# Optimization experiments

Hardware: AMD Instinct MI355X
Metric: run time of the kernel (lower is better)

Reference implementation:

```python
import jax, jax.numpy as jnp
import numpy as np

N_X, N_NEIGH, D_IN, D_HID, D_OUT = 8192, 8192, 512, 32, 256
NEG_BIG = -9.0e15


def setup_inputs() -> dict:
    key = jax.random.key(0)
    ks = jax.random.split(key, 16)
    s_in = 1.0 / np.sqrt(D_IN)
    s_hid = 1.0 / np.sqrt(D_HID)
    return {
        "x": jax.random.normal(ks[0], (N_X, D_IN), jnp.float32),
        "neigh": jax.random.normal(ks[1], (N_NEIGH, D_IN), jnp.float32),
        "adj": jax.random.randint(ks[2], (N_X, N_NEIGH), 0, 2, jnp.int32),
        # att_x MLP: Linear(D_IN,D_HID) -> tanh -> Linear(D_HID,D_HID)
        "Wx1": jax.random.uniform(ks[3], (D_IN, D_HID), jnp.float32, -s_in, s_in),
        "bx1": jnp.zeros((D_HID,), jnp.float32),
        "Wx2": jax.random.uniform(ks[4], (D_HID, D_HID), jnp.float32, -s_hid, s_hid),
        "bx2": jnp.zeros((D_HID,), jnp.float32),
        # att_neigh MLP
        "Wn1": jax.random.uniform(ks[5], (D_IN, D_HID), jnp.float32, -s_in, s_in),
        "bn1": jnp.zeros((D_HID,), jnp.float32),
        "Wn2": jax.random.uniform(ks[6], (D_HID, D_HID), jnp.float32, -s_hid, s_hid),
        "bn2": jnp.zeros((D_HID,), jnp.float32),
        # fc_value, fc_x
        "Wv": jax.random.uniform(ks[7], (D_IN, D_OUT), jnp.float32, -s_in, s_in),
        "bv": jnp.zeros((D_OUT,), jnp.float32),
        "Wfx": jax.random.uniform(ks[8], (D_IN, D_OUT), jnp.float32, -s_in, s_in),
        "bfx": jnp.zeros((D_OUT,), jnp.float32),
    }


def reference(x, neigh, adj, Wx1, bx1, Wx2, bx2, Wn1, bn1, Wn2, bn2, Wv, bv, Wfx, bfx):
    # eval mode: dropouts are identity. edge_emb gather in original is dead code.
    neib_att = jnp.tanh(neigh @ Wn1 + bn1) @ Wn2 + bn2      # (N_neigh, H)
    value = neigh @ Wv + bv                                  # (N_neigh, D_OUT)
    x_att = jnp.tanh(x @ Wx1 + bx1) @ Wx2 + bx2              # (N_x, H)
    ws = jnp.einsum("nh,mh->nm", x_att, neib_att)            # (N_x, N_neigh)
    ws = jax.nn.leaky_relu(ws, negative_slope=0.01)
    ws = jnp.where(adj > 0, ws, jnp.float32(NEG_BIG))
    ws = jax.nn.softmax(ws, axis=1)
    agg_neib = ws @ value                                    # (N_x, D_OUT)
    out = jnp.concatenate([x @ Wfx + bfx, agg_neib], axis=1)  # (N_x, 2*D_OUT)
    return out
```

## Files before the change

### kernel.cpp

```cpp
#include <hip/hip_runtime.h>
#include <hip/hip_bf16.h>

#define NX 8192
#define NN 8192
#define DIN 512
#define DHID 32
#define DOUT 256

typedef __bf16 bf16x8 __attribute__((ext_vector_type(8)));
typedef float f32x4 __attribute__((ext_vector_type(4)));
typedef unsigned short u16x8 __attribute__((ext_vector_type(8)));

__device__ __forceinline__ unsigned short f2bf(float f) {
  __hip_bfloat16 h = __float2bfloat16(f);
  return __builtin_bit_cast(unsigned short, h);
}
__device__ __forceinline__ float bf2f(unsigned short u) {
  unsigned int v = ((unsigned int)u) << 16;
  return __builtin_bit_cast(float, v);
}
__device__ __forceinline__ f32x4 mfma16(u16x8 a, u16x8 b, f32x4 c) {
  return __builtin_amdgcn_mfma_f32_16x16x32_bf16(
      __builtin_bit_cast(bf16x8, a), __builtin_bit_cast(bf16x8, b), c, 0, 0, 0);
}
__device__ __forceinline__ u16x8 cvt8(float4 a0, float4 a1) {
  u16x8 u;
  u[0] = f2bf(a0.x); u[1] = f2bf(a0.y); u[2] = f2bf(a0.z); u[3] = f2bf(a0.w);
  u[4] = f2bf(a1.x); u[5] = f2bf(a1.y); u[6] = f2bf(a1.z); u[7] = f2bf(a1.w);
  return u;
}

__global__ __launch_bounds__(256) void k_wt(
    const float* __restrict__ Wv, const float* __restrict__ Wfx,
    const float* __restrict__ Wx1, const float* __restrict__ Wn1,
    const float* __restrict__ Wx2, const float* __restrict__ Wn2,
    unsigned short* __restrict__ WvT, unsigned short* __restrict__ WfxT,
    unsigned short* __restrict__ Wx1T, unsigned short* __restrict__ Wn1T,
    unsigned short* __restrict__ Wx2T, unsigned short* __restrict__ Wn2T) {
  const float* src; unsigned short* dst; int K, C;
  switch (blockIdx.y) {
    case 0:  src = Wv;  dst = WvT;  K = DIN; C = 256; break;
    case 1:  src = Wfx; dst = WfxT; K = DIN; C = 256; break;
    case 2:  src = Wx1; dst = Wx1T; K = DIN; C = 32;  break;
    case 3:  src = Wn1; dst = Wn1T; K = DIN; C = 32;  break;
    case 4:  src = Wx2; dst = Wx2T; K = 32;  C = 32;  break;
    default: src = Wn2; dst = Wn2T; K = 32;  C = 32;  break;
  }
  int tc = C >> 5, tk = K >> 5;
  if ((int)blockIdx.x >= tc * tk) return;
  int ik = blockIdx.x / tc, ic = blockIdx.x % tc;
  __shared__ float tile[32][33];
  int t = threadIdx.x, tx = t & 31, ty0 = t >> 5;
  #pragma unroll
  for (int q = 0; q < 4; ++q) {
    int ty = ty0 + q * 8;
    tile[ty][tx] = src[(ik * 32 + ty) * C + ic * 32 + tx];
  }
  __syncthreads();
  #pragma unroll
  for (int q = 0; q < 4; ++q) {
    int ty = ty0 + q * 8;
    dst[(ic * 32 + ty) * K + ik * 32 + tx] = f2bf(tile[tx][ty]);
  }
}

__global__ __launch_bounds__(256) void k_prep(
    const float* __restrict__ x, const float* __restrict__ neigh,
    const float* __restrict__ bfx, const float* __restrict__ bv,
    const float* __restrict__ bx1, const float* __restrict__ bn1,
    const unsigned short* __restrict__ WfxT, const unsigned short* __restrict__ WvT,
    const unsigned short* __restrict__ Wx1T, const unsigned short* __restrict__ Wn1T,
    float* __restrict__ out, unsigned short* __restrict__ Vp,
    unsigned short* __restrict__ Hx, unsigned short* __restrict__ Hn) {
  int job = blockIdx.y;
  const float* A = job ? neigh : x;
  const float* bias = job ? bv : bfx;
  const float* b1 = job ? bn1 : bx1;
  const unsigned short* WT = job ? WvT : WfxT;
  const unsigned short* W1T = job ? Wn1T : Wx1T;
  unsigned short* H = job ? Hn : Hx;
  __shared__ __align__(16) char As[2][64 * 64];
  int t = threadIdx.x;
  int lane = t & 63, w = t >> 6;
  int r = lane & 15, h4 = lane >> 4;
  int bm = blockIdx.x * 64;
  f32x4 acc[4][4];
  f32x4 acch[4];
  #pragma unroll
  for (int i = 0; i < 4; ++i) {
    acch[i] = (f32x4){0.f, 0.f, 0.f, 0.f};
    #pragma unroll
    for (int j = 0; j < 4; ++j) acc[i][j] = (f32x4){0.f, 0.f, 0.f, 0.f};
  }
  int srow = t >> 2, kq = t & 3;
  const float* ap = A + (long)(bm + srow) * DIN + kq * 8;
  float4 a0 = *reinterpret_cast<const float4*>(ap);
  float4 a1 = *reinterpret_cast<const float4*>(ap + 4);
  u16x8 pbc[4], pbhc;
  #pragma unroll
  for (int nt = 0; nt < 4; ++nt)
    pbc[nt] = *reinterpret_cast<const u16x8*>(WT + (w * 64 + nt * 16 + r) * DIN + h4 * 8);
  if (w < 2)
    pbhc = *reinterpret_cast<const u16x8*>(W1T + (w * 16 + r) * DIN + h4 * 8);
  int boff = (srow * 64 + kq * 16) ^ ((srow & 3) << 4);
  int buf = 0;
  for (int kk = 0; kk < 16; ++kk) {
    u16x8 u = cvt8(a0, a1);
    *reinterpret_cast<u16x8*>(&As[buf][0] + boff) = u;
    __syncthreads();
    u16x8 pbn[4], pbhn;
    if (kk < 15) {
      a0 = *reinterpret_cast<const float4*>(ap + (kk + 1) * 32);
      a1 = *reinterpret_cast<const float4*>(ap + (kk + 1) * 32 + 4);
      #pragma unroll
      for (int nt = 0; nt < 4; ++nt)
        pbn[nt] = *reinterpret_cast<const u16x8*>(
            WT + (w * 64 + nt * 16 + r) * DIN + (kk + 1) * 32 + h4 * 8);
      if (w < 2)
        pbhn = *reinterpret_cast<const u16x8*>(
            W1T + (w * 16 + r) * DIN + (kk + 1) * 32 + h4 * 8);
    }
    #pragma unroll
    for (int mt = 0; mt < 4; ++mt) {
      int ro = mt * 16 + r;
      int aoff = (ro * 64 + h4 * 16) ^ ((ro & 3) << 4);
      u16x8 pa = *reinterpret_cast<const u16x8*>(&As[buf][0] + aoff);
      #pragma unroll
      for (int nt = 0; nt < 4; ++nt) acc[mt][nt] = mfma16(pa, pbc[nt], acc[mt][nt]);
      if (w < 2) acch[mt] = mfma16(pa, pbhc, acch[mt]);
    }
    #pragma unroll
    for (int nt = 0; nt < 4; ++nt) pbc[nt] = pbn[nt];
    pbhc = pbhn;
    buf ^= 1;
  }
  #pragma unroll
  for (int mt = 0; mt < 4; ++mt)
    #pragma unroll
    for (int nt = 0; nt < 4; ++nt) {
      int c = w * 64 + nt * 16 + r;
      #pragma unroll
      for (int j = 0; j < 4; ++j) {
        int row = bm + mt * 16 + h4 * 4 + j;
        float v = acc[mt][nt][j] + bias[c];
        if (job == 0) out[(long)row * 512 + c] = v;
        else Vp[((row >> 3) * 256 + c) * 8 + (row & 7)] = f2bf(v);
      }
    }
  if (w < 2) {
    int c = w * 16 + r;
    float bb = b1[c];
    #pragma unroll
    for (int mt = 0; mt < 4; ++mt)
      #pragma unroll
      for (int j = 0; j < 4; ++j) {
        int row = bm + mt * 16 + h4 * 4 + j;
        H[row * DHID + c] = f2bf(tanhf(acch[mt][j] + bb));
      }
  }
}

__global__ __launch_bounds__(256) void k_att(
    const unsigned short* __restrict__ Hx, const unsigned short* __restrict__ Hn,
    const float* __restrict__ bx2, const float* __restrict__ bn2,
    const unsigned short* __restrict__ Wx2T, const unsigned short* __restrict__ Wn2T,
    unsigned short* __restrict__ xatt, unsigned short* __restrict__ natt) {
  const unsigned short* H; const float* b2; const unsigned short* WT; unsigned short* att;
  if (blockIdx.y == 0) { H = Hx; b2 = bx2; WT = Wx2T; att = xatt; }
  else                 { H = Hn; b2 = bn2; WT = Wn2T; att = natt; }
  int lane = threadIdx.x & 63, w = threadIdx.x >> 6;
  int r = lane & 15, h4 = lane >> 4;
  int row = blockIdx.x * 64 + w * 16 + r;
  u16x8 af = *reinterpret_cast<const u16x8*>(H + row * DHID + h4 * 8);
  u16x8 b0 = *reinterpret_cast<const u16x8*>(WT + r * DHID + h4 * 8);
  u16x8 b1 = *reinterpret_cast<const u16x8*>(WT + (16 + r) * DHID + h4 * 8);
  f32x4 z = {0.f, 0.f, 0.f, 0.f};
  f32x4 acc0 = mfma16(af, b0, z);
  f32x4 acc1 = mfma16(af, b1, z);
  int orow = blockIdx.x * 64 + w * 16 + h4 * 4;
  #pragma unroll
  for (int j = 0; j < 4; ++j) {
    att[(orow + j) * DHID + r]      = f2bf(acc0[j] + b2[r]);
    att[(orow + j) * DHID + 16 + r] = f2bf(acc1[j] + b2[16 + r]);
  }
}

__global__ __launch_bounds__(1024, 2) void k_flash(
    const int* __restrict__ adj, const unsigned short* __restrict__ xatt,
    const unsigned short* __restrict__ natt, const unsigned short* __restrict__ Vp,
    float* __restrict__ out, unsigned short* __restrict__ accP,
    float* __restrict__ lP, int nc) {
  __shared__ unsigned short P[2][128 * 40];
  __shared__ __align__(16) unsigned short Vl[2][4 * 256 * 8];
  __shared__ float lpart[16][16];
  int t = threadIdx.x;
  int lane = t & 63, w = t >> 6;
  int r = lane & 15, h4 = lane >> 4;
  int rt = w >> 1, ns = w & 1;
  int fid = blockIdx.y * gridDim.x + blockIdx.x;
  int g = 8 / nc;
  int m8 = fid & 7;
  int my = m8 / g;
  int mx = (fid >> 3) * g + (m8 % g);
  int rb = mx * 128;
  int L = NN / nc;
  int base = my * L;
  int NIT = L / 32;
  int lastn = base + L - 32;
  u16x8 qf = *reinterpret_cast<const u16x8*>(xatt + (rb + rt * 16 + r) * DHID + h4 * 8);
  f32x4 o[8];
  #pragma unroll
  for (int i = 0; i < 8; ++i) o[i] = (f32x4){0.f, 0.f, 0.f, 0.f};
  float psum[4] = {0.f, 0.f, 0.f, 0.f};
  int adjA[4], adjB[4];
  u16x8 kfA, kfB;
  #pragma unroll
  for (int j = 0; j < 4; ++j) {
    long ro = (long)(rb + rt * 16 + h4 * 4 + j) * NN + ns * 16 + r;
    adjA[j] = __builtin_nontemporal_load(&adj[ro + base]);
    adjB[j] = __builtin_nontemporal_load(&adj[ro + base + 32]);
  }
  kfA = *reinterpret_cast<const u16x8*>(natt + (base + ns * 16 + r) * DHID + h4 * 8);
  kfB = *reinterpret_cast<const u16x8*>(natt + (base + 32 + ns * 16 + r) * DHID + h4 * 8);
  {
    u16x8 v0 = *reinterpret_cast<const u16x8*>(Vp + (long)base * 256 + t * 8);
    *reinterpret_cast<u16x8*>(&Vl[0][0] + t * 8) = v0;
  }
  u16x8 vregA = *reinterpret_cast<const u16x8*>(Vp + (long)(base + 32) * 256 + t * 8);
  __syncthreads();
  int pb = 0, vb = 0;
  for (int it = 0; it < NIT; ++it) {
    int n0 = base + it * 32;
    f32x4 z = {0.f, 0.f, 0.f, 0.f};
    f32x4 s = mfma16(qf, kfA, z);
    unsigned short* Pb = &P[pb][0];
    #pragma unroll
    for (int j = 0; j < 4; ++j) {
      float sv = s[j];
      float lr = fminf(fmaxf(sv, 0.01f * sv), 60.f);
      float p = (adjA[j] > 0) ? __expf(lr) : 0.f;
      psum[j] += p;
      Pb[(rt * 16 + h4 * 4 + j) * 40 + ns * 16 + r] = f2bf(p);
    }
    __syncthreads();
    #pragma unroll
    for (int j = 0; j < 4; ++j) adjA[j] = adjB[j];
    kfA = kfB;
    int nn = n0 + 64 <= lastn ? n0 + 64 : lastn;
    #pragma unroll
    for (int j = 0; j < 4; ++j)
      adjB[j] = __builtin_nontemporal_load(
          &adj[(long)(rb + rt * 16 + h4 * 4 + j) * NN + nn + ns * 16 + r]);
    kfB = *reinterpret_cast<const u16x8*>(natt + (nn + ns * 16 + r) * DHID + h4 * 8);
    u16x8 vregB = *reinterpret_cast<const u16x8*>(Vp + (long)nn * 256 + t * 8);
    u16x8 pa = *reinterpret_cast<const u16x8*>(&P[pb][0] + (rt * 16 + r) * 40 + h4 * 8);
    #pragma unroll
    for (int ct = 0; ct < 8; ++ct) {
      u16x8 vf = *reinterpret_cast<const u16x8*>(
          &Vl[vb][0] + (h4 * 256 + ns * 128 + ct * 16 + r) * 8);
      o[ct] = mfma16(pa, vf, o[ct]);
    }
    *reinterpret_cast<u16x8*>(&Vl[vb ^ 1][0] + t * 8) = vregA;
    vregA = vregB;
    pb ^= 1; vb ^= 1;
  }
  #pragma unroll
  for (int q = 1; q < 16; q <<= 1)
    #pragma unroll
    for (int j = 0; j < 4; ++j) psum[j] += __shfl_xor(psum[j], q);
  if (r == 0) {
    #pragma unroll
    for (int j = 0; j < 4; ++j) lpart[w][h4 * 4 + j] = psum[j];
  }
  __syncthreads();
  int cb = ns * 128;
  if (nc == 1) {
    #pragma unroll
    for (int ct = 0; ct < 8; ++ct) {
      int c = cb + ct * 16 + r;
      #pragma unroll
      for (int j = 0; j < 4; ++j) {
        int rl = rt * 16 + h4 * 4 + j;
        float l = lpart[2 * rt][h4 * 4 + j] + lpart[2 * rt + 1][h4 * 4 + j];
        out[(long)(rb + rl) * 512 + 256 + c] = o[ct][j] / l;
      }
    }
  } else {
    long cbase = (long)my * NX;
    #pragma unroll
    for (int ct = 0; ct < 8; ++ct) {
      int c = cb + ct * 16 + r;
      #pragma unroll
      for (int j = 0; j < 4; ++j) {
        int rl = rt * 16 + h4 * 4 + j;
        accP[(cbase + rb + rl) * DOUT + c] = f2bf(o[ct][j]);
      }
    }
    if (t < 128)
      lP[my * NX + rb + t] =
          lpart[2 * (t >> 4)][t & 15] + lpart[2 * (t >> 4) + 1][t & 15];
  }
}

__global__ __launch_bounds__(256) void k_combine(
    const unsigned short* __restrict__ accP, const float* __restrict__ lP,
    float* __restrict__ out, int nc) {
  long idx = (long)blockIdx.x * 256 + threadIdx.x;
  int row = (int)(idx >> 8), c = (int)(idx & 255);
  float s = 0.f, l = 0.f;
  for (int q = 0; q < nc; ++q) {
    s += bf2f(accP[(long)q * NX * DOUT + idx]);
    l += lP[q * NX + row];
  }
  out[(long)row * 512 + 256 + c] = s / l;
}

extern "C" void kernel_launch(void* const* d_in, const int* in_sizes, int n_in,
                              void* d_out, int out_size, void* d_ws, size_t ws_size,
                              hipStream_t stream) {
  const float* x    = (const float*)d_in[0];
  const float* neigh= (const float*)d_in[1];
  const int*   adj  = (const int*)d_in[2];
  const float* Wx1  = (const float*)d_in[3];
  const float* bx1  = (const float*)d_in[4];
  const float* Wx2  = (const float*)d_in[5];
  const float* bx2  = (const float*)d_in[6];
  const float* Wn1  = (const float*)d_in[7];
  const float* bn1  = (const float*)d_in[8];
  const float* Wn2  = (const float*)d_in[9];
  const float* bn2  = (const float*)d_in[10];
  const float* Wv   = (const float*)d_in[11];
  const float* bv   = (const float*)d_in[12];
  const float* Wfx  = (const float*)d_in[13];
  const float* bfx  = (const float*)d_in[14];
  float* out = (float*)d_out;
  char* ws = (char*)d_ws;

  unsigned short* xatt = (unsigned short*)(ws + 0);
  unsigned short* natt = (unsigned short*)(ws + 524288);
  unsigned short* Hx   = (unsigned short*)(ws + 1048576);
  unsigned short* Hn   = (unsigned short*)(ws + 1572864);
  unsigned short* Vp   = (unsigned short*)(ws + 2097152);
  unsigned short* WvT  = (unsigned short*)(ws + 6291456);
  unsigned short* WfxT = (unsigned short*)(ws + 6553600);
  unsigned short* Wx1T = (unsigned short*)(ws + 6815744);
  unsigned short* Wn1T = (unsigned short*)(ws + 6848512);
  unsigned short* Wx2T = (unsigned short*)(ws + 6881280);
  unsigned short* Wn2T = (unsigned short*)(ws + 6883328);

  const size_t OFF_ACC = 16777216;
  const size_t CHUNK_ACC = (size_t)NX * DOUT * 2;
  size_t need4 = OFF_ACC + 4 * (CHUNK_ACC + (size_t)NX * 4);
  size_t need2 = OFF_ACC + 2 * (CHUNK_ACC + (size_t)NX * 4);
  int nc = (ws_size >= need4) ? 4 : (ws_size >= need2) ? 2 : 1;
  unsigned short* accP = (unsigned short*)(ws + OFF_ACC);
  float* lP = (float*)(ws + OFF_ACC + (size_t)nc * CHUNK_ACC);

  k_wt<<<dim3(128, 6), 256, 0, stream>>>(Wv, Wfx, Wx1, Wn1, Wx2, Wn2,
                                         WvT, WfxT, Wx1T, Wn1T, Wx2T, Wn2T);
  k_prep<<<dim3(128, 2), 256, 0, stream>>>(x, neigh, bfx, bv, bx1, bn1,
                                           WfxT, WvT, Wx1T, Wn1T, out, Vp, Hx, Hn);
  k_att<<<dim3(128, 2), 256, 0, stream>>>(Hx, Hn, bx2, bn2, Wx2T, Wn2T, xatt, natt);
  k_flash<<<dim3(64, nc), 1024, 0, stream>>>(adj, xatt, natt, Vp, out, accP, lP, nc);
  if (nc > 1)
    k_combine<<<dim3(NX * DOUT / 256), 256, 0, stream>>>(accP, lP, out, nc);
}
```

Baseline: 488.5 us.

## Restructure flash kernel: per-wave full row tiles, 64-neighbor V chunks, fewer barriers

The attention-aggregation kernel now runs 512 threads, with each wave owning 16 query rows across all 256 output columns instead of splitting columns between wave pairs. V is staged in 64-neighbor chunks with one barrier per chunk instead of one per 32. The P tile is private to each wave, and adjacency is loaded as int4 vectors with the score MFMA transposed. This cuts barrier count, cross-wave softmax-sum reduction and per-element adjacency loads. In exchange it doubles the accumulator registers per wave and raises LDS use for V.

```diff
diff --git a/kernel.cpp b/kernel.cpp
--- a/kernel.cpp
+++ b/kernel.cpp
@@ -185,18 +185,16 @@
   }
 }
 
-__global__ __launch_bounds__(1024, 2) void k_flash(
+__global__ __launch_bounds__(512, 2) void k_flash(
     const int* __restrict__ adj, const unsigned short* __restrict__ xatt,
     const unsigned short* __restrict__ natt, const unsigned short* __restrict__ Vp,
     float* __restrict__ out, unsigned short* __restrict__ accP,
     float* __restrict__ lP, int nc) {
-  __shared__ unsigned short P[2][128 * 40];
-  __shared__ __align__(16) unsigned short Vl[2][4 * 256 * 8];
-  __shared__ float lpart[16][16];
+  __shared__ __align__(16) unsigned short Vl[2][64 * 256];
+  __shared__ __align__(16) unsigned short Ps[8][16 * 40];
   int t = threadIdx.x;
   int lane = t & 63, w = t >> 6;
   int r = lane & 15, h4 = lane >> 4;
-  int rt = w >> 1, ns = w & 1;
   int fid = blockIdx.y * gridDim.x + blockIdx.x;
   int g = 8 / nc;
   int m8 = fid & 7;
@@ -205,100 +203,111 @@
   int rb = mx * 128;
   int L = NN / nc;
   int base = my * L;
-  int NIT = L / 32;
-  int lastn = base + L - 32;
-  u16x8 qf = *reinterpret_cast<const u16x8*>(xatt + (rb + rt * 16 + r) * DHID + h4 * 8);
-  f32x4 o[8];
-  #pragma unroll
-  for (int i = 0; i < 8; ++i) o[i] = (f32x4){0.f, 0.f, 0.f, 0.f};
-  float psum[4] = {0.f, 0.f, 0.f, 0.f};
-  int adjA[4], adjB[4];
-  u16x8 kfA, kfB;
-  #pragma unroll
-  for (int j = 0; j < 4; ++j) {
-    long ro = (long)(rb + rt * 16 + h4 * 4 + j) * NN + ns * 16 + r;
-    adjA[j] = __builtin_nontemporal_load(&adj[ro + base]);
-    adjB[j] = __builtin_nontemporal_load(&adj[ro + base + 32]);
-  }
-  kfA = *reinterpret_cast<const u16x8*>(natt + (base + ns * 16 + r) * DHID + h4 * 8);
-  kfB = *reinterpret_cast<const u16x8*>(natt + (base + 32 + ns * 16 + r) * DHID + h4 * 8);
-  {
-    u16x8 v0 = *reinterpret_cast<const u16x8*>(Vp + (long)base * 256 + t * 8);
-    *reinterpret_cast<u16x8*>(&Vl[0][0] + t * 8) = v0;
-  }
-  u16x8 vregA = *reinterpret_cast<const u16x8*>(Vp + (long)(base + 32) * 256 + t * 8);
+  int NCH = L / 64;
+  int qrow = rb + w * 16;
+  u16x8 qf = *reinterpret_cast<const u16x8*>(xatt + (long)(qrow + r) * DHID + h4 * 8);
+  f32x4 o[16];
+  #pragma unroll
+  for (int i = 0; i < 16; ++i) o[i] = (f32x4){0.f, 0.f, 0.f, 0.f};
+  float psum = 0.f;
+  const int* ap = adj + (long)(qrow + r) * NN + h4 * 4;
+  u16x8 vs[4], vs2[4];
+  #pragma unroll
+  for (int q = 0; q < 4; ++q)
+    vs[q] = *reinterpret_cast<const u16x8*>(Vp + (long)base * 256 + (q * 512 + t) * 8);
+  int4 ajA[2], ajB[2];
+  u16x8 kfA[2], kfB[2];
+  #pragma unroll
+  for (int h = 0; h < 2; ++h) {
+    ajA[h] = *reinterpret_cast<const int4*>(ap + base + h * 16);
+    ajB[h] = *reinterpret_cast<const int4*>(ap + base + 32 + h * 16);
+    kfA[h] = *reinterpret_cast<const u16x8*>(natt + (long)(base + h * 16 + r) * DHID + h4 * 8);
+    kfB[h] = *reinterpret_cast<const u16x8*>(natt + (long)(base + 32 + h * 16 + r) * DHID + h4 * 8);
+  }
+  #pragma unroll
+  for (int q = 0; q < 4; ++q)
+    *reinterpret_cast<u16x8*>(&Vl[0][(q * 512 + t) * 8]) = vs[q];
+  #pragma unroll
+  for (int q = 0; q < 4; ++q)
+    vs[q] = *reinterpret_cast<const u16x8*>(
+        Vp + (long)(base + 64) * 256 + (q * 512 + t) * 8);
   __syncthreads();
-  int pb = 0, vb = 0;
-  for (int it = 0; it < NIT; ++it) {
-    int n0 = base + it * 32;
-    f32x4 z = {0.f, 0.f, 0.f, 0.f};
-    f32x4 s = mfma16(qf, kfA, z);
-    unsigned short* Pb = &P[pb][0];
-    #pragma unroll
-    for (int j = 0; j < 4; ++j) {
-      float sv = s[j];
-      float lr = fminf(fmaxf(sv, 0.01f * sv), 60.f);
-      float p = (adjA[j] > 0) ? __expf(lr) : 0.f;
-      psum[j] += p;
-      Pb[(rt * 16 + h4 * 4 + j) * 40 + ns * 16 + r] = f2bf(p);
-    }
+  int vb = 0;
+  int lastit = 2 * NCH - 1;
+  for (int c = 0; c < NCH; ++c) {
+    int c2 = c + 2 < NCH ? c + 2 : NCH - 1;
+    #pragma unroll
+    for (int q = 0; q < 4; ++q)
+      vs2[q] = *reinterpret_cast<const u16x8*>(
+          Vp + (long)(base + c2 * 64) * 256 + (q * 512 + t) * 8);
+    #pragma unroll
+    for (int q = 0; q < 4; ++q)
+      *reinterpret_cast<u16x8*>(&Vl[vb ^ 1][(q * 512 + t) * 8]) = vs[q];
+    unsigned short* Pw = &Ps[w][0];
+    const unsigned short* Vb = &Vl[vb][0];
+    #pragma unroll
+    for (int s2 = 0; s2 < 2; ++s2) {
+      int it = 2 * c + s2;
+      int itp = it + 2 <= lastit ? it + 2 : lastit;
+      int np = base + itp * 32;
+      #pragma unroll
+      for (int h = 0; h < 2; ++h) {
+        f32x4 z = {0.f, 0.f, 0.f, 0.f};
+        f32x4 s = mfma16(kfA[h], qf, z);
+        int am[4] = {ajA[h].x, ajA[h].y, ajA[h].z, ajA[h].w};
+        #pragma unroll
+        for (int j = 0; j < 4; ++j) {
+          float sv = s[j];
+          float lr = fminf(fmaxf(sv, 0.01f * sv), 60.f);
+          float p = (am[j] > 0) ? __expf(lr) : 0.f;
+          psum += p;
+          Pw[r * 40 + h * 16 + h4 * 4 + j] = f2bf(p);
+        }
+      }
+      #pragma unroll
+      for (int h = 0; h < 2; ++h) {
+        ajA[h] = ajB[h];
+        kfA[h] = kfB[h];
+        ajB[h] = *reinterpret_cast<const int4*>(ap + np + h * 16);
+        kfB[h] = *reinterpret_cast<const u16x8*>(
+            natt + (long)(np + h * 16 + r) * DHID + h4 * 8);
+      }
+      u16x8 pa = *reinterpret_cast<const u16x8*>(Pw + r * 40 + h4 * 8);
+      #pragma unroll
+      for (int ct = 0; ct < 16; ++ct) {
+        u16x8 vf = *reinterpret_cast<const u16x8*>(
+            Vb + ((s2 * 4 + h4) * 256 + ct * 16 + r) * 8);
+        o[ct] = mfma16(pa, vf, o[ct]);
+      }
+    }
+    #pragma unroll
+    for (int q = 0; q < 4; ++q) vs[q] = vs2[q];
     __syncthreads();
-    #pragma unroll
-    for (int j = 0; j < 4; ++j) adjA[j] = adjB[j];
-    kfA = kfB;
-    int nn = n0 + 64 <= lastn ? n0 + 64 : lastn;
-    #pragma unroll
-    for (int j = 0; j < 4; ++j)
-      adjB[j] = __builtin_nontemporal_load(
-          &adj[(long)(rb + rt * 16 + h4 * 4 + j) * NN + nn + ns * 16 + r]);
-    kfB = *reinterpret_cast<const u16x8*>(natt + (nn + ns * 16 + r) * DHID + h4 * 8);
-    u16x8 vregB = *reinterpret_cast<const u16x8*>(Vp + (long)nn * 256 + t * 8);
-    u16x8 pa = *reinterpret_cast<const u16x8*>(&P[pb][0] + (rt * 16 + r) * 40 + h4 * 8);
-    #pragma unroll
-    for (int ct = 0; ct < 8; ++ct) {
-      u16x8 vf = *reinterpret_cast<const u16x8*>(
-          &Vl[vb][0] + (h4 * 256 + ns * 128 + ct * 16 + r) * 8);
-      o[ct] = mfma16(pa, vf, o[ct]);
-    }
-    *reinterpret_cast<u16x8*>(&Vl[vb ^ 1][0] + t * 8) = vregA;
-    vregA = vregB;
-    pb ^= 1; vb ^= 1;
-  }
-  #pragma unroll
-  for (int q = 1; q < 16; q <<= 1)
-    #pragma unroll
-    for (int j = 0; j < 4; ++j) psum[j] += __shfl_xor(psum[j], q);
-  if (r == 0) {
-    #pragma unroll
-    for (int j = 0; j < 4; ++j) lpart[w][h4 * 4 + j] = psum[j];
-  }
-  __syncthreads();
-  int cb = ns * 128;
+    vb ^= 1;
+  }
+  psum += __shfl_xor(psum, 16);
+  psum += __shfl_xor(psum, 32);
+  float lq[4];
+  #pragma unroll
+  for (int j = 0; j < 4; ++j) lq[j] = __shfl(psum, h4 * 4 + j);
   if (nc == 1) {
     #pragma unroll
-    for (int ct = 0; ct < 8; ++ct) {
-      int c = cb + ct * 16 + r;
-      #pragma unroll
-      for (int j = 0; j < 4; ++j) {
-        int rl = rt * 16 + h4 * 4 + j;
-        float l = lpart[2 * rt][h4 * 4 + j] + lpart[2 * rt + 1][h4 * 4 + j];
-        out[(long)(rb + rl) * 512 + 256 + c] = o[ct][j] / l;
-      }
+    for (int ct = 0; ct < 16; ++ct) {
+      int cc = ct * 16 + r;
+      #pragma unroll
+      for (int j = 0; j < 4; ++j)
+        out[(long)(qrow + h4 * 4 + j) * 512 + 256 + cc] = o[ct][j] / lq[j];
     }
   } else {
-    long cbase = (long)my * NX;
-    #pragma unroll
-    for (int ct = 0; ct < 8; ++ct) {
-      int c = cb + ct * 16 + r;
-      #pragma unroll
-      for (int j = 0; j < 4; ++j) {
-        int rl = rt * 16 + h4 * 4 + j;
-        accP[(cbase + rb + rl) * DOUT + c] = f2bf(o[ct][j]);
-      }
-    }
-    if (t < 128)
-      lP[my * NX + rb + t] =
-          lpart[2 * (t >> 4)][t & 15] + lpart[2 * (t >> 4) + 1][t & 15];
+    long cb = (long)my * NX;
+    #pragma unroll
+    for (int ct = 0; ct < 16; ++ct) {
+      int cc = ct * 16 + r;
+      #pragma unroll
+      for (int j = 0; j < 4; ++j)
+        accP[(cb + qrow + h4 * 4 + j) * DOUT + cc] = f2bf(o[ct][j]);
+    }
+    if (h4 == 0) lP[my * NX + qrow + r] = psum;
   }
 }
 
@@ -361,7 +370,7 @@
   k_prep<<<dim3(128, 2), 256, 0, stream>>>(x, neigh, bfx, bv, bx1, bn1,
                                            WfxT, WvT, Wx1T, Wn1T, out, Vp, Hx, Hn);
   k_att<<<dim3(128, 2), 256, 0, stream>>>(Hx, Hn, bx2, bn2, Wx2T, Wn2T, xatt, natt);
-  k_flash<<<dim3(64, nc), 1024, 0, stream>>>(adj, xatt, natt, Vp, out, accP, lP, nc);
+  k_flash<<<dim3(64, nc), 512, 0, stream>>>(adj, xatt, natt, Vp, out, accP, lP, nc);
   if (nc > 1)
     k_combine<<<dim3(NX * DOUT / 256), 256, 0, stream>>>(accP, lP, out, nc);
 }
```

Result: faster. 461.9 us (-5.5%).
